# Kernel tuning notes

Measured on AMD Instinct MI355X. Metric: run time of the kernel, lower is better.

Reference implementation:

```python
import jax, jax.numpy as jnp
import numpy as np

S, B, V = 128, 256, 256   # seq_len, batch, vec_size
NC, R = 32, 8             # n_choices, redundancy; C = NC*R summer choices
NAND_BIAS_INIT = 4.0      # nand_weight init: ones + nand_bias(3.0)


def setup_inputs() -> dict:
    key = jax.random.key(0)
    ks = jax.random.split(key, 9)
    f = lambda k, sh: jax.random.normal(k, sh, dtype=jnp.float32)
    return {
        "attend_var": f(ks[0], (S, B, V)),
        "x_name": f(ks[1], (S, B, V)),
        "x": f(ks[2], (S, B, V)),
        "y_name": f(ks[3], (S, B, V)),
        "y": f(ks[4], (S, B, V)),
        "summer_vecs": f(ks[5], (NC, V)),
        "summer_weight": f(ks[6], (NC * R, 2 * V)),
        "summer_nand_weight": jnp.full((NC * R, 2), NAND_BIAS_INIT, dtype=jnp.float32),
        "default": f(ks[7], (4, V)),
        "var_nand_weight": jax.random.uniform(ks[8], (6, 3), dtype=jnp.float32),
    }


def _cos(a, b, eps=1e-8):
    # torch.cosine_similarity semantics: dot / max(|a||b|, eps) along last axis
    num = jnp.sum(a * b, axis=-1)
    na = jnp.maximum(jnp.linalg.norm(a, axis=-1), eps)
    nb = jnp.maximum(jnp.linalg.norm(b, axis=-1), eps)
    return num / (na * nb)


def reference(attend_var, x_name, x, y_name, y, summer_vecs, summer_weight,
              summer_nand_weight, default, var_nand_weight):
    Wq = summer_weight.reshape(NC * R, 2, V)        # [C, 2, V]
    nw_s = jax.nn.sigmoid(summer_nand_weight)       # [C, 2]
    nw_v = jax.nn.sigmoid(var_nand_weight)          # [6, 3]

    def step(running_sum, inp):
        av, xn, xv, yn, yv = inp                    # each [B, V]
        bsz = av.shape[0]
        # FwdNAND over 3 cosine similarities -> [B, 6] choice weights
        cs = jnp.stack([_cos(av, xn), _cos(av, yn), _cos(xn, yn)], axis=1)  # [B,3]
        interp = nw_v[None] * cs[:, None, :] + (1.0 - nw_v[None]) * (1.0 - cs[:, None, :])
        var_choice = jnp.prod(interp, axis=2)       # [B, 6]
        # choose among x, y, and 4 default vectors
        cands = jnp.concatenate(
            [xv[:, None, :], yv[:, None, :], jnp.broadcast_to(default[None], (bsz, 4, V))],
            axis=1)                                  # [B, 6, V]
        val = jnp.einsum('bc,bcv->bv', var_choice, cands)
        # NAND summer: cos sim of (running_sum, val) against C weight pairs
        q = jnp.stack([running_sum, val], axis=1)   # [B, 2, V]
        cs2 = _cos(q[:, None, :, :], Wq[None, :, :, :])  # [B, C, 2]
        cs2 = jax.nn.leaky_relu(cs2)                # clip='leaky_relu'
        interp2 = nw_s[None] * cs2 + (1.0 - nw_s[None]) * (1.0 - cs2)
        choices = jnp.prod(interp2, axis=2)         # [B, C]
        new_rs = jnp.einsum('cv,bcr->bv', summer_vecs, choices.reshape(bsz, NC, R))
        return new_rs, new_rs

    rs0 = jnp.zeros((attend_var.shape[1], V), dtype=attend_var.dtype) + 1e-6
    _, outs = jax.lax.scan(step, rs0, (attend_var, x_name, x, y_name, y))
    return jnp.transpose(outs, (1, 0, 2))           # [B, S, V]
```

## Files before the change

### kernel.cpp

```cpp
#include <hip/hip_runtime.h>
#include <hip/hip_fp16.h>
#include <math.h>


namespace {

constexpr float EPS = 1e-8f;

typedef _Float16 half8  __attribute__((ext_vector_type(8)));
typedef __fp16   fp16x2 __attribute__((ext_vector_type(2)));
typedef float    f32x4  __attribute__((ext_vector_type(4)));

__device__ __forceinline__ float sigmoidf_(float x) {
    return 1.0f / (1.0f + expf(-x));
}

#define RTREE64(p) do { \
    p += __shfl_xor(p, 32); p += __shfl_xor(p, 16); p += __shfl_xor(p, 8); \
    p += __shfl_xor(p, 4);  p += __shfl_xor(p, 2);  p += __shfl_xor(p, 1); } while (0)

#define RED32(p) do { \
    p += __shfl_xor(p, 16); p += __shfl_xor(p, 8); \
    p += __shfl_xor(p, 4);  p += __shfl_xor(p, 2);  p += __shfl_xor(p, 1); } while (0)

#define DPP_ADD(x, CTRL) \
    ((x) + __int_as_float(__builtin_amdgcn_mov_dpp( \
        __float_as_int(x), (CTRL), 0xF, 0xF, true)))
#define DPP_MOVF(x, CTRL) \
    __int_as_float(__builtin_amdgcn_mov_dpp(__float_as_int(x), (CTRL), 0xF, 0xF, true))
#define RDLANE(x, L) \
    __int_as_float(__builtin_amdgcn_readlane(__float_as_int(x), (L)))

#define REP32(F) F(0) F(1) F(2) F(3) F(4) F(5) F(6) F(7) \
                 F(8) F(9) F(10) F(11) F(12) F(13) F(14) F(15) \
                 F(16) F(17) F(18) F(19) F(20) F(21) F(22) F(23) \
                 F(24) F(25) F(26) F(27) F(28) F(29) F(30) F(31)
#define REP16(F) F(0) F(1) F(2) F(3) F(4) F(5) F(6) F(7) \
                 F(8) F(9) F(10) F(11) F(12) F(13) F(14) F(15)

#define DOT8(A0, A1, B0, B1) \
    ((A0).x * (B0).x + (A0).y * (B0).y + (A0).z * (B0).z + (A0).w * (B0).w + \
     (A1).x * (B1).x + (A1).y * (B1).y + (A1).z * (B1).z + (A1).w * (B1).w)

#define PACK8(DST, U, W)                                           \
    do {                                                           \
        union { fp16x2 p[4]; uint4 q; } pk_;                       \
        pk_.p[0] = __builtin_amdgcn_cvt_pkrtz((U).x, (U).y);       \
        pk_.p[1] = __builtin_amdgcn_cvt_pkrtz((U).z, (U).w);       \
        pk_.p[2] = __builtin_amdgcn_cvt_pkrtz((W).x, (W).y);       \
        pk_.p[3] = __builtin_amdgcn_cvt_pkrtz((W).z, (W).w);       \
        *reinterpret_cast<uint4*>(DST) = pk_.q;                    \
    } while (0)

__device__ __forceinline__ unsigned pk2u(float a, float b) {
    union { fp16x2 p; unsigned u; } cv;
    cv.p = __builtin_amdgcn_cvt_pkrtz(a, b);
    return cv.u;
}

__global__ void __launch_bounds__(256) prep_kernel(
    const float* __restrict__ sv, const float* __restrict__ sw,
    const float* __restrict__ snw, const float* __restrict__ def,
    const float* __restrict__ vnw,
    float* __restrict__ M0T, unsigned* __restrict__ M0Tp,
    float* __restrict__ PD, float* __restrict__ G,
    float* __restrict__ w0s, float* __restrict__ iw0, float* __restrict__ iw1,
    float* __restrict__ n0, float* __restrict__ n1,
    float* __restrict__ nwv_g, float* __restrict__ DD_g)
{
    const int t = threadIdx.x, wave = t >> 6, lane = t & 63;
    __shared__ float wsum[39][4];

    if (blockIdx.x < 256) {
        const int c = blockIdx.x;
        const float w0v = sw[(size_t)c * 512 + t];
        const float w1v = sw[(size_t)c * 512 + 256 + t];
#pragma unroll
        for (int k = 0; k < 32; ++k) {
            float p = w0v * sv[k * 256 + t];
            RTREE64(p);
            if (lane == 0) wsum[k][wave] = p;
        }
#pragma unroll
        for (int j = 0; j < 4; ++j) {
            float p = w1v * def[j * 256 + t];
            RTREE64(p);
            if (lane == 0) wsum[32 + j][wave] = p;
        }
        {
            float p = w0v * w0v; RTREE64(p); if (lane == 0) wsum[36][wave] = p;
            float q = w1v * w1v; RTREE64(q); if (lane == 0) wsum[37][wave] = q;
            float r = w0v;       RTREE64(r); if (lane == 0) wsum[38][wave] = r;
        }
        __syncthreads();
        if (t < 32) {
            const float v = wsum[t][0] + wsum[t][1] + wsum[t][2] + wsum[t][3];
            M0T[t * 256 + c] = v;
            const float vn = __shfl_down(v, 1);
            if ((t & 1) == 0)
                M0Tp[c * 16 + (t >> 1)] = pk2u(v, vn);
        } else if (t < 36) {
            PD[(t - 32) * 256 + c] =
                wsum[t][0] + wsum[t][1] + wsum[t][2] + wsum[t][3];
        } else if (t == 36) {
            iw0[c] = 1.0f / fmaxf(sqrtf(wsum[36][0] + wsum[36][1] +
                                        wsum[36][2] + wsum[36][3]), EPS);
        } else if (t == 37) {
            iw1[c] = 1.0f / fmaxf(sqrtf(wsum[37][0] + wsum[37][1] +
                                        wsum[37][2] + wsum[37][3]), EPS);
        } else if (t == 38) {
            w0s[c] = wsum[38][0] + wsum[38][1] + wsum[38][2] + wsum[38][3];
        } else if (t == 39) {
            n0[c] = sigmoidf_(snw[2 * c]);
        } else if (t == 40) {
            n1[c] = sigmoidf_(snw[2 * c + 1]);
        }
    } else if (blockIdx.x < 288) {
        const int k = blockIdx.x - 256;
        const float svk = sv[k * 256 + t];
#pragma unroll
        for (int m = 0; m < 32; ++m) {
            float p = svk * sv[m * 256 + t];
            RTREE64(p);
            if (lane == 0) wsum[m][wave] = p;
        }
        __syncthreads();
        if (t < 32)
            G[k * 32 + t] = wsum[t][0] + wsum[t][1] + wsum[t][2] + wsum[t][3];
    } else {
        const float dv0 = def[t], dv1 = def[256 + t];
        const float dv2 = def[512 + t], dv3 = def[768 + t];
        float dv[4] = {dv0, dv1, dv2, dv3};
#pragma unroll
        for (int i = 0; i < 4; ++i) {
#pragma unroll
            for (int j = 0; j < 4; ++j) {
                float p = dv[i] * dv[j];
                RTREE64(p);
                if (lane == 0) wsum[i * 4 + j][wave] = p;
            }
        }
        __syncthreads();
        if (t < 16)
            DD_g[t] = wsum[t][0] + wsum[t][1] + wsum[t][2] + wsum[t][3];
        if (t >= 32 && t < 50)
            nwv_g[t - 32] = sigmoidf_(vnw[t - 32]);
    }
}

__global__ void __launch_bounds__(256) stats_kernel(
    const float* __restrict__ x, const float* __restrict__ y,
    const float* __restrict__ av_g, const float* __restrict__ xn_g,
    const float* __restrict__ yn_g, const float* __restrict__ def,
    const float* __restrict__ sw, const float* __restrict__ nwv_g,
    const float* __restrict__ DD_g,
    __half* __restrict__ xh, __half* __restrict__ yh,
    __half* __restrict__ swh, float* __restrict__ coef_g)
{
    const int blk = blockIdx.x;
    const int t   = threadIdx.x;

    if (blk >= 4096) {
        const size_t j = ((size_t)(blk - 4096) * 256 + t) * 8;
        const int c = (int)(j >> 8), k = (int)(j & 255);
        const float* src = sw + (size_t)c * 512 + 256 + k;
        const float4 u = *(const float4*)(src);
        const float4 w = *(const float4*)(src + 4);
        PACK8(swh + j, u, w);
        return;
    }

    const int seg = t >> 5;
    const int li  = t & 31;
    const int m   = blk * 8 + seg;
    const int v0  = li * 8;
    const size_t base = (size_t)m * 256 + v0;

    const float4 xa = *(const float4*)(x + base);
    const float4 xb = *(const float4*)(x + base + 4);
    const float4 ya = *(const float4*)(y + base);
    const float4 yb = *(const float4*)(y + base + 4);
    const float4 aa = *(const float4*)(av_g + base);
    const float4 ab = *(const float4*)(av_g + base + 4);
    const float4 na = *(const float4*)(xn_g + base);
    const float4 nb = *(const float4*)(xn_g + base + 4);
    const float4 ma = *(const float4*)(yn_g + base);
    const float4 mb = *(const float4*)(yn_g + base + 4);

    PACK8(xh + base, xa, xb);
    PACK8(yh + base, ya, yb);

    float r0 = DOT8(aa, ab, na, nb);
    float r1 = DOT8(aa, ab, ma, mb);
    float r2 = DOT8(na, nb, ma, mb);
    float r3 = DOT8(aa, ab, aa, ab);
    float r4 = DOT8(na, nb, na, nb);
    float r5 = DOT8(ma, mb, ma, mb);
    float r6 = DOT8(xa, xb, xa, xb);
    float r7 = DOT8(ya, yb, ya, yb);
    float r8 = DOT8(xa, xb, ya, yb);
    float r9, r10, r11, r12, r13, r14, r15, r16;
    {
        const float4 d0a = *(const float4*)(def + v0);
        const float4 d0b = *(const float4*)(def + v0 + 4);
        r9  = DOT8(xa, xb, d0a, d0b);  r13 = DOT8(ya, yb, d0a, d0b);
        const float4 d1a = *(const float4*)(def + 256 + v0);
        const float4 d1b = *(const float4*)(def + 256 + v0 + 4);
        r10 = DOT8(xa, xb, d1a, d1b);  r14 = DOT8(ya, yb, d1a, d1b);
        const float4 d2a = *(const float4*)(def + 512 + v0);
        const float4 d2b = *(const float4*)(def + 512 + v0 + 4);
        r11 = DOT8(xa, xb, d2a, d2b);  r15 = DOT8(ya, yb, d2a, d2b);
        const float4 d3a = *(const float4*)(def + 768 + v0);
        const float4 d3b = *(const float4*)(def + 768 + v0 + 4);
        r12 = DOT8(xa, xb, d3a, d3b);  r16 = DOT8(ya, yb, d3a, d3b);
    }
    RED32(r0);  RED32(r1);  RED32(r2);  RED32(r3);  RED32(r4);  RED32(r5);
    RED32(r6);  RED32(r7);  RED32(r8);  RED32(r9);  RED32(r10); RED32(r11);
    RED32(r12); RED32(r13); RED32(r14); RED32(r15); RED32(r16);

    const float nav = fmaxf(sqrtf(r3), EPS);
    const float nxn = fmaxf(sqrtf(r4), EPS);
    const float nyn = fmaxf(sqrtf(r5), EPS);
    float cs[3];
    cs[0] = r0 / (nav * nxn);
    cs[1] = r1 / (nav * nyn);
    cs[2] = r2 / (nxn * nyn);

    float vc[6];
#pragma unroll
    for (int jj = 0; jj < 6; ++jj) {
        float p = 1.0f;
#pragma unroll
        for (int k = 0; k < 3; ++k) {
            const float a = nwv_g[jj * 3 + k];
            p = p * (a * cs[k] + (1.0f - a) * (1.0f - cs[k]));
        }
        vc[jj] = p;
    }

    float val2 = vc[0] * vc[0] * r6 + vc[1] * vc[1] * r7
               + 2.0f * vc[0] * vc[1] * r8;
    const float sx = vc[2] * r9  + vc[3] * r10 + vc[4] * r11 + vc[5] * r12;
    const float sy = vc[2] * r13 + vc[3] * r14 + vc[4] * r15 + vc[5] * r16;
    val2 += 2.0f * vc[0] * sx + 2.0f * vc[1] * sy;
#pragma unroll
    for (int i2 = 0; i2 < 4; ++i2) {
#pragma unroll
        for (int j2 = 0; j2 < 4; ++j2) {
            val2 += vc[2 + i2] * vc[2 + j2] * DD_g[i2 * 4 + j2];
        }
    }
    const float inv_val = 1.0f / fmaxf(sqrtf(val2), EPS);

    if (li == 0) {
        const float4 cA = {vc[0] * inv_val, vc[1] * inv_val,
                           vc[2] * inv_val, vc[3] * inv_val};
        const float4 cB = {vc[4] * inv_val, vc[5] * inv_val, 0.f, 0.f};
        *(float4*)(coef_g + (size_t)m * 8)     = cA;
        *(float4*)(coef_g + (size_t)m * 8 + 4) = cB;
    }
}

__global__ void __launch_bounds__(256) pxy_gemm(
    const __half* __restrict__ xh, const __half* __restrict__ yh,
    const __half* __restrict__ swh, __half* __restrict__ pxy)
{
    const int swz      = (blockIdx.x & 7) * 256 + (blockIdx.x >> 3);
    const int cstrip   = swz & 7;
    const int rowblock = swz >> 3;
    const int wid  = threadIdx.x >> 6;
    const int lane = threadIdx.x & 63;
    const int l16  = lane & 15;
    const int lhi  = lane >> 4;
    const bool isx = rowblock < 128;
    const __half* __restrict__ A = isx ? xh : yh;
    const int row0   = (isx ? rowblock : rowblock - 128) * 256 + wid * 64;
    const int cbase  = cstrip * 32;
    const int colout = isx ? 0 : 256;

    const f32x4 z = {0.f, 0.f, 0.f, 0.f};
    f32x4 acc00 = z, acc01 = z, acc10 = z, acc11 = z;
    f32x4 acc20 = z, acc21 = z, acc30 = z, acc31 = z;

    const __half* arow = A   + (size_t)(row0 + l16) * 256;
    const __half* brow = swh + (size_t)(cbase + l16) * 256;

#pragma unroll
    for (int k0 = 0; k0 < 256; k0 += 32) {
        const int ka = k0 + lhi * 8;
        const half8 a0 = *(const half8*)(arow + ka);
        const half8 a1 = *(const half8*)(arow + 16 * 256 + ka);
        const half8 a2 = *(const half8*)(arow + 32 * 256 + ka);
        const half8 a3 = *(const half8*)(arow + 48 * 256 + ka);
        const half8 b0 = *(const half8*)(brow + ka);
        const half8 b1 = *(const half8*)(brow + 16 * 256 + ka);
        acc00 = __builtin_amdgcn_mfma_f32_16x16x32_f16(a0, b0, acc00, 0, 0, 0);
        acc01 = __builtin_amdgcn_mfma_f32_16x16x32_f16(a0, b1, acc01, 0, 0, 0);
        acc10 = __builtin_amdgcn_mfma_f32_16x16x32_f16(a1, b0, acc10, 0, 0, 0);
        acc11 = __builtin_amdgcn_mfma_f32_16x16x32_f16(a1, b1, acc11, 0, 0, 0);
        acc20 = __builtin_amdgcn_mfma_f32_16x16x32_f16(a2, b0, acc20, 0, 0, 0);
        acc21 = __builtin_amdgcn_mfma_f32_16x16x32_f16(a2, b1, acc21, 0, 0, 0);
        acc30 = __builtin_amdgcn_mfma_f32_16x16x32_f16(a3, b0, acc30, 0, 0, 0);
        acc31 = __builtin_amdgcn_mfma_f32_16x16x32_f16(a3, b1, acc31, 0, 0, 0);
    }

    const int colp = (((colout + cbase) >> 5) << 4) + l16;
#define STPAIR(ACCA, ACCB, ROFF)                                          \
    do {                                                                  \
        union { fp16x2 p[4]; uint4 u; } pk;                               \
        pk.p[0] = __builtin_amdgcn_cvt_pkrtz((ACCA)[0], (ACCA)[1]);       \
        pk.p[1] = __builtin_amdgcn_cvt_pkrtz((ACCA)[2], (ACCA)[3]);       \
        pk.p[2] = __builtin_amdgcn_cvt_pkrtz((ACCB)[0], (ACCB)[1]);       \
        pk.p[3] = __builtin_amdgcn_cvt_pkrtz((ACCB)[2], (ACCB)[3]);       \
        const size_t hb = (size_t)(((row0 + (ROFF)) >> 2) + lhi) * 2048   \
                        + (size_t)colp * 8;                               \
        *reinterpret_cast<uint4*>(pxy + hb) = pk.u;                       \
    } while (0)
    STPAIR(acc00, acc01, 0);
    STPAIR(acc10, acc11, 16);
    STPAIR(acc20, acc21, 32);
    STPAIR(acc30, acc31, 48);
#undef STPAIR
}

__device__ __forceinline__ float half_of(uint2 u, int j) {
    const unsigned w = (j < 2) ? u.x : u.y;
    const unsigned sh = (unsigned)(j & 1) * 16u;
    return __half2float(__ushort_as_half((unsigned short)(w >> sh)));
}

__global__ void __launch_bounds__(256) finish_kernel(
    const float* __restrict__ coef_g, const float* __restrict__ PD_g,
    const float* __restrict__ iw1_g, const float* __restrict__ n1_g,
    const __half* __restrict__ pxy, float* __restrict__ i1_g)
{
    const int mg = blockIdx.x;
    const int t = threadIdx.x;

    const int cpx = ((t >> 5) << 4) + (t & 15);
    const int ppx = (t >> 4) & 1;
    const size_t gb = (size_t)mg * 2048;
    const uint2 upx = *reinterpret_cast<const uint2*>(
        pxy + gb + (size_t)cpx * 8 + ppx * 4);
    const uint2 upy = *reinterpret_cast<const uint2*>(
        pxy + gb + (size_t)(128 + cpx) * 8 + ppx * 4);

    const float pd0 = PD_g[t],        pd1 = PD_g[256 + t];
    const float pd2 = PD_g[512 + t],  pd3 = PD_g[768 + t];
    const float iw1v = iw1_g[t];
    const float n1v  = n1_g[t];
    const float An = 2.0f * n1v - 1.0f;
    const float Bn = 1.0f - n1v;

#pragma unroll
    for (int j = 0; j < 4; ++j) {
        const int m = 4 * mg + j;
        const float4 cA = *(const float4*)(coef_g + (size_t)m * 8);
        const float2 cB = *(const float2*)(coef_g + (size_t)m * 8 + 4);
        const float px = half_of(upx, j);
        const float py = half_of(upy, j);
        const float d1s = cA.x * px + cA.y * py
                        + cA.z * pd0 + cA.w * pd1 + cB.x * pd2 + cB.y * pd3;
        float c1 = d1s * iw1v;
        c1 = fmaxf(c1, 0.01f * c1);
        i1_g[(size_t)m * 256 + t] = fmaf(c1, An, Bn);
    }
}

__global__ void __launch_bounds__(64)
__attribute__((amdgpu_waves_per_eu(1, 1)))
scan_kernel(
    const float* __restrict__ i1_g, const unsigned* __restrict__ M0Tp_g,
    const float* __restrict__ G_g, const float* __restrict__ w0s_g,
    const float* __restrict__ iw0_g, const float* __restrict__ n0_g,
    float* __restrict__ gws_g)
{
    const int b = blockIdx.x;
    const int L = threadIdx.x;
    const int mcol = L >> 1;

#define LW(Q, J) uint4 W##Q##J;                                        \
    asm volatile("global_load_dwordx4 %0, %1, off"                     \
                 : "=v"(W##Q##J)                                       \
                 : "v"(M0Tp_g + ((4 * L + (Q)) * 16 + 4 * (J))));
    LW(0,0) LW(0,1) LW(0,2) LW(0,3)
    LW(1,0) LW(1,1) LW(1,2) LW(1,3)
    LW(2,0) LW(2,1) LW(2,2) LW(2,3)
    LW(3,0) LW(3,1) LW(3,2) LW(3,3)
#undef LW
#define LGF(K) float gf##K;                                            \
    asm volatile("global_load_dword %0, %1, off"                       \
                 : "=v"(gf##K) : "v"(G_g + (K) * 32 + mcol));
    REP32(LGF)
#undef LGF
    asm volatile("s_waitcnt vmcnt(0)");
    __builtin_amdgcn_sched_barrier(0);
#define PKG(J, A, B) const unsigned GP##J = pk2u(gf##A, gf##B);
    PKG(0, 0, 1)   PKG(1, 2, 3)   PKG(2, 4, 5)   PKG(3, 6, 7)
    PKG(4, 8, 9)   PKG(5, 10, 11) PKG(6, 12, 13) PKG(7, 14, 15)
    PKG(8, 16, 17) PKG(9, 18, 19) PKG(10, 20, 21) PKG(11, 22, 23)
    PKG(12, 24, 25) PKG(13, 26, 27) PKG(14, 28, 29) PKG(15, 30, 31)
#undef PKG

    const float4 w0s4 = *(const float4*)(w0s_g + 4 * L);
    const float4 iw4  = *(const float4*)(iw0_g + 4 * L);
    const float4 n04  = *(const float4*)(n0_g + 4 * L);
    const float4 di = {1e-6f * w0s4.x, 1e-6f * w0s4.y,
                       1e-6f * w0s4.z, 1e-6f * w0s4.w};
    const float4 An = {2.f * n04.x - 1.f, 2.f * n04.y - 1.f,
                       2.f * n04.z - 1.f, 2.f * n04.w - 1.f};
    const float4 Bn = {1.f - n04.x, 1.f - n04.y, 1.f - n04.z, 1.f - n04.w};

    float4 iB = *(const float4*)(i1_g + ((size_t)0 * 256 + b) * 256 + 4 * L);
    float4 iC = *(const float4*)(i1_g + ((size_t)1 * 256 + b) * 256 + 4 * L);

    float gwv;

#define NAND_GW(D0, D1, D2, D3, INV, IC)                              \
    do {                                                              \
        float cc0 = (D0) * (INV) * iw4.x; cc0 = fmaxf(cc0, 0.01f * cc0); \
        float cc1 = (D1) * (INV) * iw4.y; cc1 = fmaxf(cc1, 0.01f * cc1); \
        float cc2 = (D2) * (INV) * iw4.z; cc2 = fmaxf(cc2, 0.01f * cc2); \
        float cc3 = (D3) * (INV) * iw4.w; cc3 = fmaxf(cc3, 0.01f * cc3); \
        const float ch0 = fmaf(cc0, An.x, Bn.x) * (IC).x;             \
        const float ch1 = fmaf(cc1, An.y, Bn.y) * (IC).y;             \
        const float ch2 = fmaf(cc2, An.z, Bn.z) * (IC).z;             \
        const float ch3 = fmaf(cc3, An.w, Bn.w) * (IC).w;             \
        const float s4 = (ch0 + ch1) + (ch2 + ch3);                   \
        gwv = DPP_ADD(s4, 0xB1);        \
    } while (0)

    {
        const float inv_rs = 1.0f / fmaxf(sqrtf(2.56e-10f), EPS);
        NAND_GW(di.x, di.y, di.z, di.w, inv_rs, iB);
        if ((L & 1) == 0) gws_g[(size_t)b * 32 + mcol] = gwv;
    }
    iB = iC;

#define DOT2A(ACC, W, S) \
    asm("v_dot2_f32_f16 %0, %1, %2, %0" : "+v"(ACC) : "v"(W), "s"(S));

    for (int s = 1; s < 128; ++s) {
        const int sp = (s + 1 < 128) ? s + 1 : 127;
        const float4 iN = *(const float4*)(
            i1_g + ((size_t)sp * 256 + b) * 256 + 4 * L);

        const float tsh = DPP_MOVF(gwv, 0x4E);
        const unsigned pg = pk2u(gwv, tsh);
#define RLP(J) const unsigned sg##J = \
        (unsigned)__builtin_amdgcn_readlane((int)pg, 4 * (J));
        REP16(RLP)
#undef RLP

        float d0 = 0.f, d1 = 0.f, d2 = 0.f, d3 = 0.f, h = 0.f;
#define DQ4(ACC, WQJ, S0, S1, S2, S3)        \
        DOT2A(ACC, (WQJ).x, S0)              \
        DOT2A(ACC, (WQJ).y, S1)              \
        DOT2A(ACC, (WQJ).z, S2)              \
        DOT2A(ACC, (WQJ).w, S3)
        DQ4(d0, W00, sg0, sg1, sg2, sg3)   DQ4(d0, W01, sg4, sg5, sg6, sg7)
        DQ4(d0, W02, sg8, sg9, sg10, sg11) DQ4(d0, W03, sg12, sg13, sg14, sg15)
        DQ4(d1, W10, sg0, sg1, sg2, sg3)   DQ4(d1, W11, sg4, sg5, sg6, sg7)
        DQ4(d1, W12, sg8, sg9, sg10, sg11) DQ4(d1, W13, sg12, sg13, sg14, sg15)
        DQ4(d2, W20, sg0, sg1, sg2, sg3)   DQ4(d2, W21, sg4, sg5, sg6, sg7)
        DQ4(d2, W22, sg8, sg9, sg10, sg11) DQ4(d2, W23, sg12, sg13, sg14, sg15)
        DQ4(d3, W30, sg0, sg1, sg2, sg3)   DQ4(d3, W31, sg4, sg5, sg6, sg7)
        DQ4(d3, W32, sg8, sg9, sg10, sg11) DQ4(d3, W33, sg12, sg13, sg14, sg15)
#undef DQ4
        DOT2A(h, GP0, sg0)   DOT2A(h, GP1, sg1)   DOT2A(h, GP2, sg2)
        DOT2A(h, GP3, sg3)   DOT2A(h, GP4, sg4)   DOT2A(h, GP5, sg5)
        DOT2A(h, GP6, sg6)   DOT2A(h, GP7, sg7)   DOT2A(h, GP8, sg8)
        DOT2A(h, GP9, sg9)   DOT2A(h, GP10, sg10) DOT2A(h, GP11, sg11)
        DOT2A(h, GP12, sg12) DOT2A(h, GP13, sg13) DOT2A(h, GP14, sg14)
        DOT2A(h, GP15, sg15)

        float rp = h * gwv;
        rp = DPP_ADD(rp, 0x128);
        rp = DPP_ADD(rp, 0x124);
        rp = DPP_ADD(rp, 0x122);
        rp = DPP_ADD(rp, 0x121);
        const float rs2 = 0.5f * (RDLANE(rp, 0) + RDLANE(rp, 16) +
                                  RDLANE(rp, 32) + RDLANE(rp, 48));
        const float inv_rs = 1.0f / fmaxf(sqrtf(rs2), EPS);

        NAND_GW(d0, d1, d2, d3, inv_rs, iB);
        if ((L & 1) == 0)
            gws_g[((size_t)s * 256 + b) * 32 + mcol] = gwv;

        iB = iN;
    }
#undef DOT2A
#undef NAND_GW
}

__global__ void __launch_bounds__(256) expand_kernel(
    const float* __restrict__ gws_g, const float* __restrict__ sv_g,
    float* __restrict__ out)
{
    const int t = threadIdx.x;
    const int m0 = blockIdx.x * 32;
    __shared__ __align__(16) float SvT[256 * 36];
    __shared__ __align__(16) float gwl[32 * 32];

    for (int i = t; i < 8192; i += 256) {
        const int k = i >> 8, v = i & 255;
        SvT[v * 36 + k] = sv_g[i];
    }
    for (int i = t; i < 1024; i += 256)
        gwl[i] = gws_g[(size_t)m0 * 32 + i];
    __syncthreads();

#pragma unroll 4
    for (int r = 0; r < 32; ++r) {
        float acc = 0.f;
#pragma unroll
        for (int j = 0; j < 8; ++j) {
            const float4 g   = *(const float4*)(gwl + r * 32 + 4 * j);
            const float4 sv4 = *(const float4*)(SvT + t * 36 + 4 * j);
            acc += g.x * sv4.x + g.y * sv4.y + g.z * sv4.z + g.w * sv4.w;
        }
        const int m = m0 + r;
        const int s = m >> 8, bb = m & 255;
        out[((size_t)bb * 128 + s) * 256 + t] = acc;
    }
}

}

extern "C" void kernel_launch(void* const* d_in, const int* in_sizes, int n_in,
                              void* d_out, int out_size, void* d_ws, size_t ws_size,
                              hipStream_t stream) {
    (void)in_sizes; (void)n_in; (void)out_size; (void)ws_size;
    const float* av  = (const float*)d_in[0];
    const float* xnm = (const float*)d_in[1];
    const float* x   = (const float*)d_in[2];
    const float* ynm = (const float*)d_in[3];
    const float* y   = (const float*)d_in[4];
    const float* sv  = (const float*)d_in[5];
    const float* sw  = (const float*)d_in[6];
    const float* snw = (const float*)d_in[7];
    const float* def = (const float*)d_in[8];
    const float* vnw = (const float*)d_in[9];

    __half* pxy = (__half*)d_ws;
    float*  i1  = (float*)((char*)d_ws + (size_t)33554432);
    float*  gws = i1 + 8388608;
    float*  sm  = gws + 1048576;
    float* M0T = sm;
    float* PD  = M0T + 8192;
    float* G   = PD + 1024;
    float* w0s = G + 1024;
    float* iw0 = w0s + 256;
    float* iw1 = iw0 + 256;
    float* n0  = iw1 + 256;
    float* n1  = n0 + 256;
    unsigned* M0Tp = (unsigned*)(n1 + 256);
    __half* swh  = (__half*)(M0Tp + 4096);
    float* nwvS  = (float*)(swh + 65536);
    float* DDs   = nwvS + 32;
    float* coef  = DDs + 32;
    __half* xh = (__half*)i1;
    __half* yh = xh + 8388608;

    prep_kernel<<<dim3(289), dim3(256), 0, stream>>>(
        sv, sw, snw, def, vnw, M0T, M0Tp, PD, G, w0s, iw0, iw1, n0, n1,
        nwvS, DDs);
    stats_kernel<<<dim3(4128), dim3(256), 0, stream>>>(
        x, y, av, xnm, ynm, def, sw, nwvS, DDs, xh, yh, swh, coef);
    pxy_gemm<<<dim3(2048), dim3(256), 0, stream>>>(xh, yh, swh, pxy);
    finish_kernel<<<dim3(8192), dim3(256), 0, stream>>>(
        coef, PD, iw1, n1, pxy, i1);
    scan_kernel<<<dim3(256), dim3(64), 0, stream>>>(
        i1, M0Tp, G, w0s, iw0, n0, gws);
    expand_kernel<<<dim3(1024), dim3(256), 0, stream>>>(gws, sv, (float*)d_out);
}
```

Baseline: 192.9 us.

## Compute value norm directly, use DPP reductions, deepen recurrence prefetch

Replaces the expanded Gram-matrix formula for the norm of the chosen value with a direct per-element computation of the weighted sum followed by a squared-sum reduction. This removes the 11 extra dot products and the default-vector Gram precompute (DD_g is now zeroed and unused). Cross-lane reductions now use DPP row shifts plus a single shuffle instead of five shuffles. In the sequential recurrence kernel, the per-step input loads are prefetched three steps ahead instead of one, to hide more global-load latency at the cost of extra registers.

```diff
diff --git a/kernel.cpp b/kernel.cpp
--- a/kernel.cpp
+++ b/kernel.cpp
@@ -17,10 +17,6 @@
 
 #define RTREE64(p) do { \
     p += __shfl_xor(p, 32); p += __shfl_xor(p, 16); p += __shfl_xor(p, 8); \
-    p += __shfl_xor(p, 4);  p += __shfl_xor(p, 2);  p += __shfl_xor(p, 1); } while (0)
-
-#define RED32(p) do { \
-    p += __shfl_xor(p, 16); p += __shfl_xor(p, 8); \
     p += __shfl_xor(p, 4);  p += __shfl_xor(p, 2);  p += __shfl_xor(p, 1); } while (0)
 
 #define DPP_ADD(x, CTRL) \
@@ -30,6 +26,11 @@
     __int_as_float(__builtin_amdgcn_mov_dpp(__float_as_int(x), (CTRL), 0xF, 0xF, true))
 #define RDLANE(x, L) \
     __int_as_float(__builtin_amdgcn_readlane(__float_as_int(x), (L)))
+
+#define RED32F(p) do { \
+    p = DPP_ADD(p, 0x128); p = DPP_ADD(p, 0x124); \
+    p = DPP_ADD(p, 0x122); p = DPP_ADD(p, 0x121); \
+    p += __shfl_xor(p, 16); } while (0)
 
 #define REP32(F) F(0) F(1) F(2) F(3) F(4) F(5) F(6) F(7) \
                  F(8) F(9) F(10) F(11) F(12) F(13) F(14) F(15) \
@@ -128,23 +129,8 @@
         if (t < 32)
             G[k * 32 + t] = wsum[t][0] + wsum[t][1] + wsum[t][2] + wsum[t][3];
     } else {
-        const float dv0 = def[t], dv1 = def[256 + t];
-        const float dv2 = def[512 + t], dv3 = def[768 + t];
-        float dv[4] = {dv0, dv1, dv2, dv3};
-#pragma unroll
-        for (int i = 0; i < 4; ++i) {
-#pragma unroll
-            for (int j = 0; j < 4; ++j) {
-                float p = dv[i] * dv[j];
-                RTREE64(p);
-                if (lane == 0) wsum[i * 4 + j][wave] = p;
-            }
-        }
-        __syncthreads();
-        if (t < 16)
-            DD_g[t] = wsum[t][0] + wsum[t][1] + wsum[t][2] + wsum[t][3];
-        if (t >= 32 && t < 50)
-            nwv_g[t - 32] = sigmoidf_(vnw[t - 32]);
+        if (t < 18) nwv_g[t] = sigmoidf_(vnw[t]);
+        if (t < 16) DD_g[t] = 0.f;
     }
 }
 
@@ -157,6 +143,7 @@
     __half* __restrict__ xh, __half* __restrict__ yh,
     __half* __restrict__ swh, float* __restrict__ coef_g)
 {
+    (void)DD_g;
     const int blk = blockIdx.x;
     const int t   = threadIdx.x;
 
@@ -196,27 +183,8 @@
     float r3 = DOT8(aa, ab, aa, ab);
     float r4 = DOT8(na, nb, na, nb);
     float r5 = DOT8(ma, mb, ma, mb);
-    float r6 = DOT8(xa, xb, xa, xb);
-    float r7 = DOT8(ya, yb, ya, yb);
-    float r8 = DOT8(xa, xb, ya, yb);
-    float r9, r10, r11, r12, r13, r14, r15, r16;
-    {
-        const float4 d0a = *(const float4*)(def + v0);
-        const float4 d0b = *(const float4*)(def + v0 + 4);
-        r9  = DOT8(xa, xb, d0a, d0b);  r13 = DOT8(ya, yb, d0a, d0b);
-        const float4 d1a = *(const float4*)(def + 256 + v0);
-        const float4 d1b = *(const float4*)(def + 256 + v0 + 4);
-        r10 = DOT8(xa, xb, d1a, d1b);  r14 = DOT8(ya, yb, d1a, d1b);
-        const float4 d2a = *(const float4*)(def + 512 + v0);
-        const float4 d2b = *(const float4*)(def + 512 + v0 + 4);
-        r11 = DOT8(xa, xb, d2a, d2b);  r15 = DOT8(ya, yb, d2a, d2b);
-        const float4 d3a = *(const float4*)(def + 768 + v0);
-        const float4 d3b = *(const float4*)(def + 768 + v0 + 4);
-        r12 = DOT8(xa, xb, d3a, d3b);  r16 = DOT8(ya, yb, d3a, d3b);
-    }
-    RED32(r0);  RED32(r1);  RED32(r2);  RED32(r3);  RED32(r4);  RED32(r5);
-    RED32(r6);  RED32(r7);  RED32(r8);  RED32(r9);  RED32(r10); RED32(r11);
-    RED32(r12); RED32(r13); RED32(r14); RED32(r15); RED32(r16);
+    RED32F(r0); RED32F(r1); RED32F(r2);
+    RED32F(r3); RED32F(r4); RED32F(r5);
 
     const float nav = fmaxf(sqrtf(r3), EPS);
     const float nxn = fmaxf(sqrtf(r4), EPS);
@@ -238,18 +206,33 @@
         vc[jj] = p;
     }
 
-    float val2 = vc[0] * vc[0] * r6 + vc[1] * vc[1] * r7
-               + 2.0f * vc[0] * vc[1] * r8;
-    const float sx = vc[2] * r9  + vc[3] * r10 + vc[4] * r11 + vc[5] * r12;
-    const float sy = vc[2] * r13 + vc[3] * r14 + vc[4] * r15 + vc[5] * r16;
-    val2 += 2.0f * vc[0] * sx + 2.0f * vc[1] * sy;
-#pragma unroll
-    for (int i2 = 0; i2 < 4; ++i2) {
-#pragma unroll
-        for (int j2 = 0; j2 < 4; ++j2) {
-            val2 += vc[2 + i2] * vc[2 + j2] * DD_g[i2 * 4 + j2];
-        }
-    }
+    const float4 d0a = *(const float4*)(def + v0);
+    const float4 d0b = *(const float4*)(def + v0 + 4);
+    const float4 d1a = *(const float4*)(def + 256 + v0);
+    const float4 d1b = *(const float4*)(def + 256 + v0 + 4);
+    const float4 d2a = *(const float4*)(def + 512 + v0);
+    const float4 d2b = *(const float4*)(def + 512 + v0 + 4);
+    const float4 d3a = *(const float4*)(def + 768 + v0);
+    const float4 d3b = *(const float4*)(def + 768 + v0 + 4);
+
+    float val2 = 0.f;
+#define VALC(COMP, XA, YA, D0, D1, D2, D3)                           \
+    do {                                                             \
+        const float v_ = vc[0] * (XA).COMP + vc[1] * (YA).COMP       \
+                       + vc[2] * (D0).COMP + vc[3] * (D1).COMP       \
+                       + vc[4] * (D2).COMP + vc[5] * (D3).COMP;      \
+        val2 = fmaf(v_, v_, val2);                                   \
+    } while (0)
+    VALC(x, xa, ya, d0a, d1a, d2a, d3a);
+    VALC(y, xa, ya, d0a, d1a, d2a, d3a);
+    VALC(z, xa, ya, d0a, d1a, d2a, d3a);
+    VALC(w, xa, ya, d0a, d1a, d2a, d3a);
+    VALC(x, xb, yb, d0b, d1b, d2b, d3b);
+    VALC(y, xb, yb, d0b, d1b, d2b, d3b);
+    VALC(z, xb, yb, d0b, d1b, d2b, d3b);
+    VALC(w, xb, yb, d0b, d1b, d2b, d3b);
+#undef VALC
+    RED32F(val2);
     const float inv_val = 1.0f / fmaxf(sqrtf(val2), EPS);
 
     if (li == 0) {
@@ -411,8 +394,10 @@
                        2.f * n04.z - 1.f, 2.f * n04.w - 1.f};
     const float4 Bn = {1.f - n04.x, 1.f - n04.y, 1.f - n04.z, 1.f - n04.w};
 
-    float4 iB = *(const float4*)(i1_g + ((size_t)0 * 256 + b) * 256 + 4 * L);
-    float4 iC = *(const float4*)(i1_g + ((size_t)1 * 256 + b) * 256 + 4 * L);
+    float4 iA = *(const float4*)(i1_g + ((size_t)0 * 256 + b) * 256 + 4 * L);
+    float4 iB = *(const float4*)(i1_g + ((size_t)1 * 256 + b) * 256 + 4 * L);
+    float4 iC = *(const float4*)(i1_g + ((size_t)2 * 256 + b) * 256 + 4 * L);
+    float4 iD = *(const float4*)(i1_g + ((size_t)3 * 256 + b) * 256 + 4 * L);
 
     float gwv;
 
@@ -432,16 +417,15 @@
 
     {
         const float inv_rs = 1.0f / fmaxf(sqrtf(2.56e-10f), EPS);
-        NAND_GW(di.x, di.y, di.z, di.w, inv_rs, iB);
+        NAND_GW(di.x, di.y, di.z, di.w, inv_rs, iA);
         if ((L & 1) == 0) gws_g[(size_t)b * 32 + mcol] = gwv;
     }
-    iB = iC;
 
 #define DOT2A(ACC, W, S) \
     asm("v_dot2_f32_f16 %0, %1, %2, %0" : "+v"(ACC) : "v"(W), "s"(S));
 
     for (int s = 1; s < 128; ++s) {
-        const int sp = (s + 1 < 128) ? s + 1 : 127;
+        const int sp = (s + 3 < 128) ? s + 3 : 127;
         const float4 iN = *(const float4*)(
             i1_g + ((size_t)sp * 256 + b) * 256 + 4 * L);
 
@@ -487,7 +471,7 @@
         if ((L & 1) == 0)
             gws_g[((size_t)s * 256 + b) * 32 + mcol] = gwv;
 
-        iB = iN;
+        iB = iC; iC = iD; iD = iN;
     }
 #undef DOT2A
 #undef NAND_GW
```

Measured after the change: 192.5 us. Within noise of the previous version (-0.3%).
